# Kernel optimization log

Measured on AMD Instinct MI355X. Metric: run time of the kernel, lower is better.

## Reference

```python
import jax, jax.numpy as jnp
import numpy as np
from jax import lax

DIM = 1024
N = 8192

def setup_inputs() -> dict:
    key = jax.random.key(0)
    ks = jax.random.split(key, 7)
    ifeats = jax.random.normal(ks[0], (N, DIM), dtype=jnp.float32)
    tfeat_n = jax.random.normal(ks[1], (1, DIM), dtype=jnp.float32)
    tfeat_a = jax.random.normal(ks[2], (1, DIM), dtype=jnp.float32)
    # Conv2d(1, 2, kernel_size=(3,5), padding=(0,2)) params, OIHW
    fan_in_c = 1 * 3 * 5
    bc = 1.0 / np.sqrt(fan_in_c)
    conv_w = jax.random.uniform(ks[3], (2, 1, 3, 5), minval=-bc, maxval=bc, dtype=jnp.float32)
    conv_b = jax.random.uniform(ks[4], (2,), minval=-bc, maxval=bc, dtype=jnp.float32)
    # Linear(2*dim, dim)
    bl = 1.0 / np.sqrt(2 * DIM)
    w2 = jax.random.uniform(ks[5], (DIM, 2 * DIM), minval=-bl, maxval=bl, dtype=jnp.float32)
    b2 = jax.random.uniform(ks[6], (DIM,), minval=-bl, maxval=bl, dtype=jnp.float32)
    return {"ifeats": ifeats, "tfeat_n": tfeat_n, "tfeat_a": tfeat_a,
            "conv_w": conv_w, "conv_b": conv_b, "w2": w2, "b2": b2}

def reference(ifeats, tfeat_n, tfeat_a, conv_w, conv_b, w2, b2):
    n, d = ifeats.shape
    # Batch the per-sample loop: feats_i = [tfeat_n; tfeat_a; ifeats[i]] -> [N,1,3,D]
    tn = jnp.broadcast_to(tfeat_n, (n, d))
    ta = jnp.broadcast_to(tfeat_a, (n, d))
    x1 = jnp.stack([tn, ta, ifeats], axis=1)[:, None]  # [N,1,3,D]
    # Conv2d(1->2, k=(3,5), pad=(0,2)): height collapses 3->1, width D preserved
    x2 = lax.conv_general_dilated(x1, conv_w, window_strides=(1, 1),
                                  padding=((0, 0), (2, 2)),
                                  dimension_numbers=("NCHW", "OIHW", "NCHW"))
    x2 = x2 + conv_b[None, :, None, None]              # [N,2,1,D]
    x2 = jax.nn.gelu(x2, approximate=False)            # torch nn.GELU() is exact
    x2 = x2.reshape(n, 2 * d)                          # channel-major flatten, matches view(1,-1)
    x3 = x2 @ w2.T + b2                                # Linear(2D -> D)
    return ifeats + x3
```

## Files before the change

### kernel.cpp

```cpp
#include <hip/hip_runtime.h>
#include <cstdint>

#define DIMD 1024
#define NROWS 8192
#define KDIM 2048

typedef unsigned short u16;
typedef __bf16 bf16x8 __attribute__((ext_vector_type(8)));
typedef float f32x4 __attribute__((ext_vector_type(4)));

__device__ __forceinline__ u16 f2bf(float f) {
  unsigned u = __builtin_bit_cast(unsigned, f);
  return (u16)((u + 0x7FFFu + ((u >> 16) & 1u)) >> 16);
}

__device__ __forceinline__ float gelu_exact(float x) {
  float s = 0.70710678118654752f * x;
  float a = fabsf(s);
  float k = __fdividef(1.0f, fmaf(0.3275911f, a, 1.0f));
  float p = 1.061405429f;
  p = fmaf(p, k, -1.453152027f);
  p = fmaf(p, k, 1.421413741f);
  p = fmaf(p, k, -0.284496736f);
  p = fmaf(p, k, 0.254829592f);
  p = p * k;
  float e = __expf(-s * s);
  float erf_s = copysignf(fmaf(-p, e, 1.0f), s);
  return 0.5f * x * (1.0f + erf_s);
}

__global__ __launch_bounds__(256) void pre_kernel(
    const float* __restrict__ ifeats, const float* __restrict__ tn,
    const float* __restrict__ ta, const float* __restrict__ cw,
    const float* __restrict__ cb, const float* __restrict__ w2,
    u16* __restrict__ x2, u16* __restrict__ w2b) {
  const int b = blockIdx.x;
  const int t = threadIdx.x;
  if (b < NROWS) {
    __shared__ float si[DIMD], sn[DIMD], sa[DIMD];
    ((float4*)si)[t] = ((const float4*)(ifeats + (size_t)b * DIMD))[t];
    ((float4*)sn)[t] = ((const float4*)tn)[t];
    ((float4*)sa)[t] = ((const float4*)ta)[t];
    __syncthreads();
    const int c = t >> 7;
    const int w0 = (t & 127) << 3;
    float cwn[5], cwa[5], cwi[5];
#pragma unroll
    for (int k = 0; k < 5; ++k) {
      cwn[k] = cw[c * 15 + k];
      cwa[k] = cw[c * 15 + 5 + k];
      cwi[k] = cw[c * 15 + 10 + k];
    }
    const float bias = cb[c];
    float wn[12], wa[12], wi[12];
#pragma unroll
    for (int j = 0; j < 12; ++j) {
      int wp = w0 - 2 + j;
      bool ok = (wp >= 0) && (wp < DIMD);
      wn[j] = ok ? sn[wp] : 0.f;
      wa[j] = ok ? sa[wp] : 0.f;
      wi[j] = ok ? si[wp] : 0.f;
    }
    union { u16 o[8]; uint4 u; } pk;
#pragma unroll
    for (int s = 0; s < 8; ++s) {
      float x = bias;
#pragma unroll
      for (int k = 0; k < 5; ++k) {
        x = fmaf(cwn[k], wn[s + k], x);
        x = fmaf(cwa[k], wa[s + k], x);
        x = fmaf(cwi[k], wi[s + k], x);
      }
      pk.o[s] = f2bf(gelu_exact(x));
    }
    *(uint4*)(x2 + (size_t)b * KDIM + c * DIMD + w0) = pk.u;
  } else {
    const int t2 = (b - NROWS) * 256 + t;
    const float4* p = (const float4*)(w2 + (size_t)t2 * 8);
    float4 a = p[0], bb = p[1];
    union { u16 o[8]; uint4 v; } pk;
    pk.o[0] = f2bf(a.x);  pk.o[1] = f2bf(a.y);  pk.o[2] = f2bf(a.z);  pk.o[3] = f2bf(a.w);
    pk.o[4] = f2bf(bb.x); pk.o[5] = f2bf(bb.y); pk.o[6] = f2bf(bb.z); pk.o[7] = f2bf(bb.w);
    *(uint4*)(w2b + (size_t)t2 * 8) = pk.v;
  }
}

__device__ __forceinline__ void gl_lds16(const u16* g, u16* l) {
  __builtin_amdgcn_global_load_lds(
      (__attribute__((address_space(1))) void*)g,
      (__attribute__((address_space(3))) void*)l, 16, 0, 0);
}

#define BK 64

__global__ __launch_bounds__(512, 4) void gemm_bt(
    const u16* __restrict__ A,
    const u16* __restrict__ B,
    const float* __restrict__ ifeats,
    const float* __restrict__ b2,
    float* __restrict__ out) {
  constexpr int K = KDIM;
  __shared__ __align__(16) u16 sA[2][128 * BK];
  __shared__ __align__(16) u16 sB[2][128 * BK];

  const int tid = threadIdx.x;
  const int wv = tid >> 6;
  const int lane = tid & 63;
  const int id = blockIdx.x;
  const int xcd = id & 7;
  const int s_ = id >> 3;
  const int i0 = (xcd * 8 + (s_ >> 3)) * 128;
  const int j0 = (s_ & 7) * 128;

  const int wm = (wv & 1) * 64;
  const int wn = (wv >> 1) * 32;
  const int quad = lane >> 4;
  const int r16 = lane & 15;
  const int sw = r16 & 7;

  const int srow = lane >> 3;
  const int schunk = (lane & 7) ^ srow;
  const u16* gA[2];
  const u16* gB[2];
#pragma unroll
  for (int i = 0; i < 2; ++i) {
    int r = wv * 16 + i * 8 + srow;
    gA[i] = A + (size_t)(i0 + r) * K + schunk * 8;
    gB[i] = B + (size_t)(j0 + r) * K + schunk * 8;
  }

  const f32x4 vzero = {0.f, 0.f, 0.f, 0.f};
  f32x4 acc[4][2];
#pragma unroll
  for (int a = 0; a < 4; ++a)
#pragma unroll
    for (int b = 0; b < 2; ++b) acc[a][b] = vzero;

  auto stage = [&](int buf, int k0) {
#pragma unroll
    for (int i = 0; i < 2; ++i) {
      u16* la = &sA[buf][(wv * 16 + i * 8) * BK];
      u16* lb = &sB[buf][(wv * 16 + i * 8) * BK];
      gl_lds16(gA[i] + k0, la);
      gl_lds16(gB[i] + k0, lb);
    }
  };

  auto compute = [&](int buf) {
#pragma unroll
    for (int s = 0; s < 2; ++s) {
      bf16x8 av[4], bv[2];
#pragma unroll
      for (int mt = 0; mt < 4; ++mt)
        av[mt] = *(const bf16x8*)&sA[buf][(wm + mt * 16 + r16) * BK + (((s * 4 + quad) ^ sw) << 3)];
#pragma unroll
      for (int nt = 0; nt < 2; ++nt)
        bv[nt] = *(const bf16x8*)&sB[buf][(wn + nt * 16 + r16) * BK + (((s * 4 + quad) ^ sw) << 3)];
#pragma unroll
      for (int mt = 0; mt < 4; ++mt)
#pragma unroll
        for (int nt = 0; nt < 2; ++nt)
          acc[mt][nt] = __builtin_amdgcn_mfma_f32_16x16x32_bf16(av[mt], bv[nt], acc[mt][nt], 0, 0, 0);
    }
  };

  stage(0, 0);
  for (int k0 = 0; k0 < K; k0 += 2 * BK) {
    __syncthreads();
    if (k0 + BK < K) stage(1, k0 + BK);
    compute(0);
    __syncthreads();
    if (k0 + 2 * BK < K) stage(0, k0 + 2 * BK);
    compute(1);
  }

#pragma unroll
  for (int nt = 0; nt < 2; ++nt) {
    int col = j0 + wn + nt * 16 + r16;
    float bias = b2[col];
#pragma unroll
    for (int mt = 0; mt < 4; ++mt) {
      int rbase = i0 + wm + mt * 16 + quad * 4;
#pragma unroll
      for (int r = 0; r < 4; ++r) {
        size_t idx = (size_t)(rbase + r) * DIMD + col;
        out[idx] = ifeats[idx] + bias + acc[mt][nt][r];
      }
    }
  }
}

extern "C" void kernel_launch(void* const* d_in, const int* in_sizes, int n_in,
                              void* d_out, int out_size, void* d_ws, size_t ws_size,
                              hipStream_t stream) {
  const float* ifeats = (const float*)d_in[0];
  const float* tn     = (const float*)d_in[1];
  const float* ta     = (const float*)d_in[2];
  const float* cw     = (const float*)d_in[3];
  const float* cb     = (const float*)d_in[4];
  const float* w2     = (const float*)d_in[5];
  const float* b2     = (const float*)d_in[6];
  float* out = (float*)d_out;

  u16* w2b = (u16*)d_ws;
  u16* x2  = (u16*)((char*)d_ws + (size_t)DIMD * KDIM * 2);

  pre_kernel<<<NROWS + (DIMD * KDIM / 8) / 256, 256, 0, stream>>>(
      ifeats, tn, ta, cw, cb, w2, x2, w2b);
  gemm_bt<<<512, 512, 0, stream>>>(x2, w2b, ifeats, b2, out);
}
```

Baseline: 161.4 us.

## Split GEMM K in halves with atomic accumulation, pre-init output in pre-kernel

The pre-kernel now writes out = ifeats + b2 for each row. The GEMM splits K into two halves across twice as many blocks, each block 256 threads with a 64x64 warp tile and BK=32, and each half adds its partial sums into the output with unsafeAtomicAdd. This aims to raise parallelism and warp-level reuse and to drop the epilogue reads of ifeats and bias. In exchange it adds atomic read-modify-write traffic on the full output, a non-deterministic order of the fp32 additions, and more synchronisation per K step because BK is smaller.

```diff
diff --git a/kernel.cpp b/kernel.cpp
--- a/kernel.cpp
+++ b/kernel.cpp
@@ -33,14 +33,19 @@
     const float* __restrict__ ifeats, const float* __restrict__ tn,
     const float* __restrict__ ta, const float* __restrict__ cw,
     const float* __restrict__ cb, const float* __restrict__ w2,
-    u16* __restrict__ x2, u16* __restrict__ w2b) {
+    const float* __restrict__ b2, u16* __restrict__ x2,
+    u16* __restrict__ w2b, float* __restrict__ out) {
   const int b = blockIdx.x;
   const int t = threadIdx.x;
   if (b < NROWS) {
     __shared__ float si[DIMD], sn[DIMD], sa[DIMD];
-    ((float4*)si)[t] = ((const float4*)(ifeats + (size_t)b * DIMD))[t];
+    float4 fi = ((const float4*)(ifeats + (size_t)b * DIMD))[t];
+    ((float4*)si)[t] = fi;
     ((float4*)sn)[t] = ((const float4*)tn)[t];
     ((float4*)sa)[t] = ((const float4*)ta)[t];
+    float4 fb = ((const float4*)b2)[t];
+    float4 fo = {fi.x + fb.x, fi.y + fb.y, fi.z + fb.z, fi.w + fb.w};
+    ((float4*)(out + (size_t)b * DIMD))[t] = fo;
     __syncthreads();
     const int c = t >> 7;
     const int w0 = (t & 127) << 3;
@@ -91,13 +96,12 @@
       (__attribute__((address_space(3))) void*)l, 16, 0, 0);
 }
 
-#define BK 64
-
-__global__ __launch_bounds__(512, 4) void gemm_bt(
+#define BK 32
+#define KHALF 1024
+
+__global__ __launch_bounds__(256, 4) void gemm_bt(
     const u16* __restrict__ A,
     const u16* __restrict__ B,
-    const float* __restrict__ ifeats,
-    const float* __restrict__ b2,
     float* __restrict__ out) {
   constexpr int K = KDIM;
   __shared__ __align__(16) u16 sA[2][128 * BK];
@@ -109,82 +113,78 @@
   const int id = blockIdx.x;
   const int xcd = id & 7;
   const int s_ = id >> 3;
-  const int i0 = (xcd * 8 + (s_ >> 3)) * 128;
-  const int j0 = (s_ & 7) * 128;
+  const int kh = s_ & 1;
+  const int t_ = s_ >> 1;
+  const int i0 = (xcd * 8 + (t_ >> 3)) * 128;
+  const int j0 = (t_ & 7) * 128;
+  const int kbase = kh * KHALF;
 
   const int wm = (wv & 1) * 64;
-  const int wn = (wv >> 1) * 32;
+  const int wn = (wv >> 1) * 64;
   const int quad = lane >> 4;
   const int r16 = lane & 15;
-  const int sw = r16 & 7;
-
-  const int srow = lane >> 3;
-  const int schunk = (lane & 7) ^ srow;
+  const int poff = ((quad ^ ((r16 >> 1) & 3)) << 3);
+
+  const int srow = lane >> 2;
+  const int g = (lane & 3) ^ ((lane >> 3) & 3);
   const u16* gA[2];
   const u16* gB[2];
 #pragma unroll
   for (int i = 0; i < 2; ++i) {
-    int r = wv * 16 + i * 8 + srow;
-    gA[i] = A + (size_t)(i0 + r) * K + schunk * 8;
-    gB[i] = B + (size_t)(j0 + r) * K + schunk * 8;
+    int r = wv * 32 + i * 16 + srow;
+    gA[i] = A + (size_t)(i0 + r) * K + kbase + g * 8;
+    gB[i] = B + (size_t)(j0 + r) * K + kbase + g * 8;
   }
 
   const f32x4 vzero = {0.f, 0.f, 0.f, 0.f};
-  f32x4 acc[4][2];
+  f32x4 acc[4][4];
 #pragma unroll
   for (int a = 0; a < 4; ++a)
 #pragma unroll
-    for (int b = 0; b < 2; ++b) acc[a][b] = vzero;
-
-  auto stage = [&](int buf, int k0) {
+    for (int b = 0; b < 4; ++b) acc[a][b] = vzero;
+
+  auto stage = [&](int buf, int koff) {
 #pragma unroll
     for (int i = 0; i < 2; ++i) {
-      u16* la = &sA[buf][(wv * 16 + i * 8) * BK];
-      u16* lb = &sB[buf][(wv * 16 + i * 8) * BK];
-      gl_lds16(gA[i] + k0, la);
-      gl_lds16(gB[i] + k0, lb);
+      gl_lds16(gA[i] + koff, &sA[buf][(wv * 32 + i * 16) * BK]);
+      gl_lds16(gB[i] + koff, &sB[buf][(wv * 32 + i * 16) * BK]);
     }
   };
 
   auto compute = [&](int buf) {
-#pragma unroll
-    for (int s = 0; s < 2; ++s) {
-      bf16x8 av[4], bv[2];
-#pragma unroll
-      for (int mt = 0; mt < 4; ++mt)
-        av[mt] = *(const bf16x8*)&sA[buf][(wm + mt * 16 + r16) * BK + (((s * 4 + quad) ^ sw) << 3)];
-#pragma unroll
-      for (int nt = 0; nt < 2; ++nt)
-        bv[nt] = *(const bf16x8*)&sB[buf][(wn + nt * 16 + r16) * BK + (((s * 4 + quad) ^ sw) << 3)];
-#pragma unroll
-      for (int mt = 0; mt < 4; ++mt)
-#pragma unroll
-        for (int nt = 0; nt < 2; ++nt)
-          acc[mt][nt] = __builtin_amdgcn_mfma_f32_16x16x32_bf16(av[mt], bv[nt], acc[mt][nt], 0, 0, 0);
-    }
+    bf16x8 av[4], bv[4];
+#pragma unroll
+    for (int mt = 0; mt < 4; ++mt)
+      av[mt] = *(const bf16x8*)&sA[buf][(wm + mt * 16 + r16) * BK + poff];
+#pragma unroll
+    for (int nt = 0; nt < 4; ++nt)
+      bv[nt] = *(const bf16x8*)&sB[buf][(wn + nt * 16 + r16) * BK + poff];
+#pragma unroll
+    for (int mt = 0; mt < 4; ++mt)
+#pragma unroll
+      for (int nt = 0; nt < 4; ++nt)
+        acc[mt][nt] = __builtin_amdgcn_mfma_f32_16x16x32_bf16(av[mt], bv[nt], acc[mt][nt], 0, 0, 0);
   };
 
   stage(0, 0);
-  for (int k0 = 0; k0 < K; k0 += 2 * BK) {
+  for (int k0 = 0; k0 < KHALF; k0 += 2 * BK) {
     __syncthreads();
-    if (k0 + BK < K) stage(1, k0 + BK);
+    if (k0 + BK < KHALF) stage(1, k0 + BK);
     compute(0);
     __syncthreads();
-    if (k0 + 2 * BK < K) stage(0, k0 + 2 * BK);
+    if (k0 + 2 * BK < KHALF) stage(0, k0 + 2 * BK);
     compute(1);
   }
 
 #pragma unroll
-  for (int nt = 0; nt < 2; ++nt) {
+  for (int nt = 0; nt < 4; ++nt) {
     int col = j0 + wn + nt * 16 + r16;
-    float bias = b2[col];
 #pragma unroll
     for (int mt = 0; mt < 4; ++mt) {
       int rbase = i0 + wm + mt * 16 + quad * 4;
 #pragma unroll
       for (int r = 0; r < 4; ++r) {
-        size_t idx = (size_t)(rbase + r) * DIMD + col;
-        out[idx] = ifeats[idx] + bias + acc[mt][nt][r];
+        unsafeAtomicAdd(&out[(size_t)(rbase + r) * DIMD + col], acc[mt][nt][r]);
       }
     }
   }
@@ -206,6 +206,6 @@
   u16* x2  = (u16*)((char*)d_ws + (size_t)DIMD * KDIM * 2);
 
   pre_kernel<<<NROWS + (DIMD * KDIM / 8) / 256, 256, 0, stream>>>(
-      ifeats, tn, ta, cw, cb, w2, x2, w2b);
-  gemm_bt<<<512, 512, 0, stream>>>(x2, w2b, ifeats, b2, out);
-}
+      ifeats, tn, ta, cw, cb, w2, b2, x2, w2b, out);
+  gemm_bt<<<1024, 256, 0, stream>>>(x2, w2b, out);
+}
```

Measured after the change: 197.5 us. 22.4% more time.

## Split K across two wave groups with 64x64 warp tiles and LDS reduction

Applied to the files above, without the earlier changes.

The 8 waves are regrouped into two K-groups of four. Each wave computes a 64x64 output tile over half of every BK=64 slice, instead of a 64x32 tile over the full slice. This halves LDS fragment reads per MFMA, since each fragment now feeds four MFMAs instead of two. In exchange it doubles the accumulator registers, which risks occupancy at launch_bounds(512,4), and it adds an LDS reduction step with extra barriers in the epilogue.

```diff
diff --git a/kernel.cpp b/kernel.cpp
--- a/kernel.cpp
+++ b/kernel.cpp
@@ -100,24 +100,26 @@
     const float* __restrict__ b2,
     float* __restrict__ out) {
   constexpr int K = KDIM;
-  __shared__ __align__(16) u16 sA[2][128 * BK];
-  __shared__ __align__(16) u16 sB[2][128 * BK];
+  __shared__ __align__(16) u16 smem[4][128 * BK];
 
   const int tid = threadIdx.x;
   const int wv = tid >> 6;
   const int lane = tid & 63;
+  const int kgrp = wv >> 2;
+  const int wq = wv & 3;
+  const int wm = (wq & 1) * 64;
+  const int wn = (wq >> 1) * 64;
+  const int quad = lane >> 4;
+  const int r16 = lane & 15;
+  const int sw = r16 & 7;
+  const int poff = (((kgrp * 4 + quad) ^ sw) << 3);
+
   const int id = blockIdx.x;
   const int xcd = id & 7;
   const int s_ = id >> 3;
   const int i0 = (xcd * 8 + (s_ >> 3)) * 128;
   const int j0 = (s_ & 7) * 128;
 
-  const int wm = (wv & 1) * 64;
-  const int wn = (wv >> 1) * 32;
-  const int quad = lane >> 4;
-  const int r16 = lane & 15;
-  const int sw = r16 & 7;
-
   const int srow = lane >> 3;
   const int schunk = (lane & 7) ^ srow;
   const u16* gA[2];
@@ -130,38 +132,33 @@
   }
 
   const f32x4 vzero = {0.f, 0.f, 0.f, 0.f};
-  f32x4 acc[4][2];
+  f32x4 acc[4][4];
 #pragma unroll
   for (int a = 0; a < 4; ++a)
 #pragma unroll
-    for (int b = 0; b < 2; ++b) acc[a][b] = vzero;
+    for (int b = 0; b < 4; ++b) acc[a][b] = vzero;
 
   auto stage = [&](int buf, int k0) {
 #pragma unroll
     for (int i = 0; i < 2; ++i) {
-      u16* la = &sA[buf][(wv * 16 + i * 8) * BK];
-      u16* lb = &sB[buf][(wv * 16 + i * 8) * BK];
-      gl_lds16(gA[i] + k0, la);
-      gl_lds16(gB[i] + k0, lb);
+      gl_lds16(gA[i] + k0, &smem[buf][(wv * 16 + i * 8) * BK]);
+      gl_lds16(gB[i] + k0, &smem[2 + buf][(wv * 16 + i * 8) * BK]);
     }
   };
 
   auto compute = [&](int buf) {
-#pragma unroll
-    for (int s = 0; s < 2; ++s) {
-      bf16x8 av[4], bv[2];
-#pragma unroll
-      for (int mt = 0; mt < 4; ++mt)
-        av[mt] = *(const bf16x8*)&sA[buf][(wm + mt * 16 + r16) * BK + (((s * 4 + quad) ^ sw) << 3)];
-#pragma unroll
-      for (int nt = 0; nt < 2; ++nt)
-        bv[nt] = *(const bf16x8*)&sB[buf][(wn + nt * 16 + r16) * BK + (((s * 4 + quad) ^ sw) << 3)];
-#pragma unroll
-      for (int mt = 0; mt < 4; ++mt)
-#pragma unroll
-        for (int nt = 0; nt < 2; ++nt)
-          acc[mt][nt] = __builtin_amdgcn_mfma_f32_16x16x32_bf16(av[mt], bv[nt], acc[mt][nt], 0, 0, 0);
-    }
+    bf16x8 av[4], bv[4];
+#pragma unroll
+    for (int mt = 0; mt < 4; ++mt)
+      av[mt] = *(const bf16x8*)&smem[buf][(wm + mt * 16 + r16) * BK + poff];
+#pragma unroll
+    for (int nt = 0; nt < 4; ++nt)
+      bv[nt] = *(const bf16x8*)&smem[2 + buf][(wn + nt * 16 + r16) * BK + poff];
+#pragma unroll
+    for (int mt = 0; mt < 4; ++mt)
+#pragma unroll
+      for (int nt = 0; nt < 4; ++nt)
+        acc[mt][nt] = __builtin_amdgcn_mfma_f32_16x16x32_bf16(av[mt], bv[nt], acc[mt][nt], 0, 0, 0);
   };
 
   stage(0, 0);
@@ -174,17 +171,33 @@
     compute(1);
   }
 
-#pragma unroll
-  for (int nt = 0; nt < 2; ++nt) {
-    int col = j0 + wn + nt * 16 + r16;
-    float bias = b2[col];
-#pragma unroll
-    for (int mt = 0; mt < 4; ++mt) {
-      int rbase = i0 + wm + mt * 16 + quad * 4;
-#pragma unroll
-      for (int r = 0; r < 4; ++r) {
-        size_t idx = (size_t)(rbase + r) * DIMD + col;
-        out[idx] = ifeats[idx] + bias + acc[mt][nt][r];
+  __syncthreads();
+  float* scr = (float*)smem;
+  if (kgrp == 1) {
+#pragma unroll
+    for (int nt = 0; nt < 4; ++nt)
+#pragma unroll
+      for (int mt = 0; mt < 4; ++mt) {
+        int idx = wq * 4096 + (nt * 16 + r16) * 64 + (((mt * 4 + quad) ^ r16) << 2);
+        *(f32x4*)&scr[idx] = acc[mt][nt];
+      }
+  }
+  __syncthreads();
+  if (kgrp == 0) {
+#pragma unroll
+    for (int nt = 0; nt < 4; ++nt) {
+      int col = j0 + wn + nt * 16 + r16;
+      float bias = b2[col];
+#pragma unroll
+      for (int mt = 0; mt < 4; ++mt) {
+        int idx = wq * 4096 + (nt * 16 + r16) * 64 + (((mt * 4 + quad) ^ r16) << 2);
+        f32x4 part = *(const f32x4*)&scr[idx];
+        int rbase = i0 + wm + mt * 16 + quad * 4;
+#pragma unroll
+        for (int r = 0; r < 4; ++r) {
+          size_t oix = (size_t)(rbase + r) * DIMD + col;
+          out[oix] = ifeats[oix] + bias + acc[mt][nt][r] + part[r];
+        }
       }
     }
   }
```

Result: no change. 163.1 us (+1.0%).

## Shrink GEMM tile to 128x64 with BK=32 and 256-thread blocks

Applied to the files above, without the earlier changes.

Changes the GEMM block tile from 128x128 (8 waves) to 128x64 (4 waves), halves the K step to 32, and doubles the grid to 1024 blocks. The LDS swizzle and global-to-LDS load mapping are rewritten to fit the narrower 64-byte rows. The aim is more resident blocks and better wave-level parallelism, paid for with more barriers per K sweep and lower B-tile reuse, since A is reloaded for every 64-column slice.

```diff
diff --git a/kernel.cpp b/kernel.cpp
--- a/kernel.cpp
+++ b/kernel.cpp
@@ -91,9 +91,9 @@
       (__attribute__((address_space(3))) void*)l, 16, 0, 0);
 }
 
-#define BK 64
-
-__global__ __launch_bounds__(512, 4) void gemm_bt(
+#define BK 32
+
+__global__ __launch_bounds__(256, 4) void gemm_bt(
     const u16* __restrict__ A,
     const u16* __restrict__ B,
     const float* __restrict__ ifeats,
@@ -101,33 +101,31 @@
     float* __restrict__ out) {
   constexpr int K = KDIM;
   __shared__ __align__(16) u16 sA[2][128 * BK];
-  __shared__ __align__(16) u16 sB[2][128 * BK];
+  __shared__ __align__(16) u16 sB[2][64 * BK];
 
   const int tid = threadIdx.x;
   const int wv = tid >> 6;
   const int lane = tid & 63;
+
   const int id = blockIdx.x;
   const int xcd = id & 7;
-  const int s_ = id >> 3;
-  const int i0 = (xcd * 8 + (s_ >> 3)) * 128;
-  const int j0 = (s_ & 7) * 128;
+  const int t_ = id >> 3;
+  const int i0 = (xcd * 8 + (t_ >> 4)) * 128;
+  const int j0 = (t_ & 15) * 64;
 
   const int wm = (wv & 1) * 64;
   const int wn = (wv >> 1) * 32;
   const int quad = lane >> 4;
   const int r16 = lane & 15;
-  const int sw = r16 & 7;
-
-  const int srow = lane >> 3;
-  const int schunk = (lane & 7) ^ srow;
+  const int poff = ((quad ^ ((r16 >> 1) & 3)) << 3);
+
+  const int srow = lane >> 2;
+  const int g = (lane & 3) ^ ((lane >> 3) & 3);
   const u16* gA[2];
-  const u16* gB[2];
-#pragma unroll
-  for (int i = 0; i < 2; ++i) {
-    int r = wv * 16 + i * 8 + srow;
-    gA[i] = A + (size_t)(i0 + r) * K + schunk * 8;
-    gB[i] = B + (size_t)(j0 + r) * K + schunk * 8;
-  }
+#pragma unroll
+  for (int i = 0; i < 2; ++i)
+    gA[i] = A + (size_t)(i0 + wv * 32 + i * 16 + srow) * K + g * 8;
+  const u16* gB = B + (size_t)(j0 + wv * 16 + srow) * K + g * 8;
 
   const f32x4 vzero = {0.f, 0.f, 0.f, 0.f};
   f32x4 acc[4][2];
@@ -138,30 +136,24 @@
 
   auto stage = [&](int buf, int k0) {
 #pragma unroll
-    for (int i = 0; i < 2; ++i) {
-      u16* la = &sA[buf][(wv * 16 + i * 8) * BK];
-      u16* lb = &sB[buf][(wv * 16 + i * 8) * BK];
-      gl_lds16(gA[i] + k0, la);
-      gl_lds16(gB[i] + k0, lb);
-    }
+    for (int i = 0; i < 2; ++i)
+      gl_lds16(gA[i] + k0, &sA[buf][(wv * 32 + i * 16) * BK]);
+    gl_lds16(gB + k0, &sB[buf][(wv * 16) * BK]);
   };
 
   auto compute = [&](int buf) {
-#pragma unroll
-    for (int s = 0; s < 2; ++s) {
-      bf16x8 av[4], bv[2];
-#pragma unroll
-      for (int mt = 0; mt < 4; ++mt)
-        av[mt] = *(const bf16x8*)&sA[buf][(wm + mt * 16 + r16) * BK + (((s * 4 + quad) ^ sw) << 3)];
+    bf16x8 av[4], bv[2];
+#pragma unroll
+    for (int mt = 0; mt < 4; ++mt)
+      av[mt] = *(const bf16x8*)&sA[buf][(wm + mt * 16 + r16) * BK + poff];
+#pragma unroll
+    for (int nt = 0; nt < 2; ++nt)
+      bv[nt] = *(const bf16x8*)&sB[buf][(wn + nt * 16 + r16) * BK + poff];
+#pragma unroll
+    for (int mt = 0; mt < 4; ++mt)
 #pragma unroll
       for (int nt = 0; nt < 2; ++nt)
-        bv[nt] = *(const bf16x8*)&sB[buf][(wn + nt * 16 + r16) * BK + (((s * 4 + quad) ^ sw) << 3)];
-#pragma unroll
-      for (int mt = 0; mt < 4; ++mt)
-#pragma unroll
-        for (int nt = 0; nt < 2; ++nt)
-          acc[mt][nt] = __builtin_amdgcn_mfma_f32_16x16x32_bf16(av[mt], bv[nt], acc[mt][nt], 0, 0, 0);
-    }
+        acc[mt][nt] = __builtin_amdgcn_mfma_f32_16x16x32_bf16(av[mt], bv[nt], acc[mt][nt], 0, 0, 0);
   };
 
   stage(0, 0);
@@ -183,8 +175,8 @@
       int rbase = i0 + wm + mt * 16 + quad * 4;
 #pragma unroll
       for (int r = 0; r < 4; ++r) {
-        size_t idx = (size_t)(rbase + r) * DIMD + col;
-        out[idx] = ifeats[idx] + bias + acc[mt][nt][r];
+        size_t oix = (size_t)(rbase + r) * DIMD + col;
+        out[oix] = ifeats[oix] + bias + acc[mt][nt][r];
       }
     }
   }
@@ -207,5 +199,5 @@
 
   pre_kernel<<<NROWS + (DIMD * KDIM / 8) / 256, 256, 0, stream>>>(
       ifeats, tn, ta, cw, cb, w2, x2, w2b);
-  gemm_bt<<<512, 512, 0, stream>>>(x2, w2b, ifeats, b2, out);
-}
+  gemm_bt<<<1024, 256, 0, stream>>>(x2, w2b, ifeats, b2, out);
+}
```

After: 176.1 us. 9.1% more time.
